# Optimization experiments

Hardware: AMD Instinct MI355X
Metric: run time of the kernel (lower is better)

The kernel has to match this reference:

```python
import jax, jax.numpy as jnp
import numpy as np

ALPHA = 0.2        # LeakyReLU negative slope
NEG_INF = -9e15    # mask value used by the torch module


def setup_inputs() -> dict:
    key = jax.random.key(0)
    ks = jax.random.split(key, 7)
    B, T, N, Cin = 4, 12, 1024, 64
    Fout, Em = 64, 16
    x = jax.random.normal(ks[0], (B, T, N, Cin), dtype=jnp.float32)
    adj = jax.random.randint(ks[1], (N, N), 0, 2, dtype=jnp.int32)
    emb1 = jax.random.normal(ks[2], (N, Em), dtype=jnp.float32)
    emb2 = jax.random.normal(ks[3], (N, Em), dtype=jnp.float32)
    W = jax.random.normal(ks[4], (Cin, Fout), dtype=jnp.float32) * (1.0 / np.sqrt(Cin))
    a = jax.random.normal(ks[5], (2 * Fout, 1), dtype=jnp.float32) * 0.1
    a2 = jax.random.normal(ks[6], (2 * Em, 1), dtype=jnp.float32) * 0.1
    return {"x": x, "adj": adj, "emb1": emb1, "emb2": emb2, "W": W, "a": a, "a2": a2}


def reference(x, adj, emb1, emb2, W, a, a2):
    B, T, N, Cin = x.shape
    Fout = W.shape[1]
    Em = emb1.shape[1]
    # Linear projection, fold batch*time: Wh [BT, N, Fout]
    Wh = jnp.einsum('btnc,cf->btnf', x, W).reshape(B * T, N, Fout)
    # Additive attention scores from node features
    s1 = Wh @ a[:Fout, 0]          # [BT, N]
    s2 = Wh @ a[Fout:, 0]          # [BT, N]
    e1 = s1[:, :, None] + s2[:, None, :]   # [BT, N, N]
    # Additive scores from static embeddings (shared across batch*time)
    f1 = emb1 @ a2[:Em, 0]         # [N]
    f2 = emb2 @ a2[Em:, 0]         # [N]
    e2 = f1[:, None] + f2[None, :]          # [N, N]
    e = jax.nn.leaky_relu(e1 + e2[None, :, :], negative_slope=ALPHA)
    # Adjacency mask + row softmax (dropout is inference no-op)
    att = jnp.where(adj[None, :, :] > 0, e, jnp.float32(NEG_INF))
    att = jax.nn.softmax(att, axis=-1)
    h_prime = att @ Wh                       # [BT, N, Fout]
    return jax.nn.elu(h_prime.reshape(B, T, N, Fout))
```

## Files before the change

### kernel.cpp

```cpp
#include <hip/hip_runtime.h>
#include <hip/hip_bf16.h>
#include <math.h>

#define BT 48
#define N 1024
#define F 64
#define CIN 64
#define EM 16
#define LRELU_A 0.2f
#define L2E 1.4426950408889634f

typedef short bf16x8 __attribute__((ext_vector_type(8)));
typedef float f32x4  __attribute__((ext_vector_type(4)));
typedef unsigned int u32x4 __attribute__((ext_vector_type(4)));

__device__ __forceinline__ unsigned short f2bf(float f) {
    unsigned int u = __float_as_uint(f);
    return (unsigned short)((u + 0x7FFFu + ((u >> 16) & 1u)) >> 16);
}

__global__ __launch_bounds__(256) void k_proj_misc(
    const float* __restrict__ x, const float* __restrict__ W,
    const float* __restrict__ a,
    const int* __restrict__ adj,
    const float* __restrict__ emb1, const float* __restrict__ emb2,
    const float* __restrict__ a2,
    unsigned short* __restrict__ WhSw,
    float* __restrict__ s1, float* __restrict__ s2,
    unsigned int* __restrict__ adjBits,
    float* __restrict__ f1, float* __restrict__ f2)
{
    const int tid = threadIdx.x;
    const int b   = blockIdx.x;

    __shared__ __align__(16) float sx[64 * 64];
    __shared__ __align__(16) float sWT[64 * 68];
    __shared__ __align__(16) unsigned short sT[64 * 80];

    const int bt  = b >> 4;
    const int n0  = (b & 15) * 64;
    const size_t grow = (size_t)bt * N + n0;

    {
        const float4* xv = (const float4*)(x + grow * CIN);
        float4* sxv = (float4*)sx;
        for (int i = tid; i < 64 * CIN / 4; i += 256) sxv[i] = xv[i];
        for (int i = tid; i < CIN * F; i += 256)
            sWT[(i & 63) * 68 + (i >> 6)] = W[i];
    }
    __syncthreads();

    const int f = tid & 63;
    const int w = tid >> 6;
    const float a1 = a[f], a2c = a[F + f];

    float acc[16];
#pragma unroll
    for (int t = 0; t < 16; ++t) acc[t] = 0.f;

    for (int cb = 0; cb < CIN; cb += 4) {
        const float4 wv = *(const float4*)&sWT[f * 68 + cb];
#pragma unroll
        for (int t = 0; t < 16; ++t) {
            const float4 xv = *(const float4*)&sx[(w * 16 + t) * 64 + cb];
            acc[t] = fmaf(xv.x, wv.x, acc[t]);
            acc[t] = fmaf(xv.y, wv.y, acc[t]);
            acc[t] = fmaf(xv.z, wv.z, acc[t]);
            acc[t] = fmaf(xv.w, wv.w, acc[t]);
        }
    }

#pragma unroll
    for (int t = 0; t < 16; ++t) {
        float v1 = acc[t] * a1;
        float v2 = acc[t] * a2c;
#pragma unroll
        for (int off = 32; off >= 1; off >>= 1) {
            v1 += __shfl_xor(v1, off, 64);
            v2 += __shfl_xor(v2, off, 64);
        }
        if (f == 0) {
            s1[grow + w * 16 + t] = v1;
            s2[grow + w * 16 + t] = v2;
        }
        sT[f * 80 + w * 16 + t] = f2bf(acc[t]);
    }
    __syncthreads();

    {
        const int ff = tid >> 2, qq = tid & 3;
        const int slot = (qq + ff) & 3;
        const int nb0 = (b & 15) * 2;
#pragma unroll
        for (int nbL = 0; nbL < 2; ++nbL) {
            const size_t dst = ((size_t)(bt * 32 + nb0 + nbL) * 64 + ff) * 32 + slot * 8;
            *(uint4*)&WhSw[dst] = *(const uint4*)&sT[ff * 80 + nbL * 32 + qq * 8];
        }
    }

    if (b < 128) {
        const int idx = b * 256 + tid;
        const int r = idx >> 5, w32 = idx & 31;
        const int* p = adj + (size_t)r * N + w32 * 32;
        unsigned int m = 0;
#pragma unroll
        for (int j = 0; j < 32; ++j) m |= (p[j] > 0 ? 1u : 0u) << j;
        adjBits[idx] = m;
    } else if (b < 132) {
        const int n = (b - 128) * 256 + tid;
        float v1 = 0.f, v2 = 0.f;
#pragma unroll
        for (int k = 0; k < EM; ++k) {
            v1 = fmaf(emb1[n * EM + k], a2[k], v1);
            v2 = fmaf(emb2[n * EM + k], a2[EM + k], v2);
        }
        f1[n] = v1; f2[n] = v2;
    }
}


#define PAIR(x1e, x1o, x2e, x2o, bit, dest) do {                           \
    float p0_ = fmaxf((x1e) * E1, (x2e) * E2);                             \
    float p1_ = fmaxf((x1o) * E1, (x2o) * E2);                             \
    p0_ = ((mb_ >> (bit)) & 1u) ? p0_ : 0.f;                               \
    p1_ = ((mb_ >> ((bit) + 1)) & 1u) ? p1_ : 0.f;                         \
    lsum += p0_ + p1_;                                                     \
    unsigned int pk_;                                                      \
    asm("v_cvt_pk_bf16_f32 %0, %1, %2" : "=v"(pk_) : "v"(p0_), "v"(p1_)); \
    dest = pk_;                                                            \
} while (0)

#define MAKE_ONE(ch, ks, Avar, abword) do {                                \
    const int jb_ = (ch) * 128 + (ks) * 32 + q * 8;                        \
    const float4 x1a_ = *(const float4*)&sX1[jb_];                         \
    const float4 x1b_ = *(const float4*)&sX1[jb_ + 4];                     \
    const float4 x2a_ = *(const float4*)&sX2[jb_];                         \
    const float4 x2b_ = *(const float4*)&sX2[jb_ + 4];                     \
    const unsigned int mb_ = ((abword) >> (q * 8)) & 0xFFu;                \
    unsigned int u0_, u1_, u2_, u3_;                                       \
    PAIR(x1a_.x, x1a_.y, x2a_.x, x2a_.y, 0, u0_);                          \
    PAIR(x1a_.z, x1a_.w, x2a_.z, x2a_.w, 2, u1_);                          \
    PAIR(x1b_.x, x1b_.y, x2b_.x, x2b_.y, 4, u2_);                          \
    PAIR(x1b_.z, x1b_.w, x2b_.z, x2b_.w, 6, u3_);                          \
    u32x4 av_; av_.x = u0_; av_.y = u1_; av_.z = u2_; av_.w = u3_;         \
    Avar = __builtin_bit_cast(bf16x8, av_);                                \
} while (0)

#define MAKE_AFR(ch, abv, A0, A1, A2, A3) do {                             \
    MAKE_ONE(ch, 0, A0, abv.x);                                            \
    MAKE_ONE(ch, 1, A1, abv.y);                                            \
    MAKE_ONE(ch, 2, A2, abv.z);                                            \
    MAKE_ONE(ch, 3, A3, abv.w);                                            \
} while (0)

#define LB(v, ch, ks, ct)                                                  \
    v = *(const bf16x8*)(gBc + (size_t)(ch) * 16384 + (ks) * 4096 +        \
        ((ct) * 16 + m15) * 64 + slotoff)

#define LOAD8(B0, B1, B2, B3, B4, B5, B6, B7, ch, ct0, ct1) do {           \
    LB(B0, ch, 0, ct0); LB(B1, ch, 1, ct0);                                \
    LB(B2, ch, 2, ct0); LB(B3, ch, 3, ct0);                                \
    LB(B4, ch, 0, ct1); LB(B5, ch, 1, ct1);                                \
    LB(B6, ch, 2, ct1); LB(B7, ch, 3, ct1);                                \
} while (0)

#define MFMA8(B0, B1, B2, B3, B4, B5, B6, B7, c0, c1) do {                 \
    acc##c0 = __builtin_amdgcn_mfma_f32_16x16x32_bf16(fA0, B0, acc##c0, 0, 0, 0); \
    acc##c0 = __builtin_amdgcn_mfma_f32_16x16x32_bf16(fA1, B1, acc##c0, 0, 0, 0); \
    acc##c0 = __builtin_amdgcn_mfma_f32_16x16x32_bf16(fA2, B2, acc##c0, 0, 0, 0); \
    acc##c0 = __builtin_amdgcn_mfma_f32_16x16x32_bf16(fA3, B3, acc##c0, 0, 0, 0); \
    acc##c1 = __builtin_amdgcn_mfma_f32_16x16x32_bf16(fA0, B4, acc##c1, 0, 0, 0); \
    acc##c1 = __builtin_amdgcn_mfma_f32_16x16x32_bf16(fA1, B5, acc##c1, 0, 0, 0); \
    acc##c1 = __builtin_amdgcn_mfma_f32_16x16x32_bf16(fA2, B6, acc##c1, 0, 0, 0); \
    acc##c1 = __builtin_amdgcn_mfma_f32_16x16x32_bf16(fA3, B7, acc##c1, 0, 0, 0); \
} while (0)

#define CHUNK_MID(ch) do {                                                 \
    LOAD8(Q0, Q1, Q2, Q3, Q4, Q5, Q6, Q7, ch, 2, 3);                       \
    const uint4 abv_ = abRow4[ch];                                         \
    MAKE_AFR(ch, abv_, fA0, fA1, fA2, fA3);                                \
    MFMA8(P0, P1, P2, P3, P4, P5, P6, P7, 0, 1);                           \
    LOAD8(P0, P1, P2, P3, P4, P5, P6, P7, (ch) + 1, 0, 1);                 \
    MFMA8(Q0, Q1, Q2, Q3, Q4, Q5, Q6, Q7, 2, 3);                           \
} while (0)

#define CHUNK_LAST(ch) do {                                                \
    LOAD8(Q0, Q1, Q2, Q3, Q4, Q5, Q6, Q7, ch, 2, 3);                       \
    const uint4 abv_ = abRow4[ch];                                         \
    MAKE_AFR(ch, abv_, fA0, fA1, fA2, fA3);                                \
    MFMA8(P0, P1, P2, P3, P4, P5, P6, P7, 0, 1);                           \
    MFMA8(Q0, Q1, Q2, Q3, Q4, Q5, Q6, Q7, 2, 3);                           \
} while (0)

#define EPI(ct, accv) do {                                                 \
    float h0_ = accv.x * rinv0, h1_ = accv.y * rinv1,                      \
          h2_ = accv.z * rinv2, h3_ = accv.w * rinv3;                      \
    h0_ = (h0_ > 0.f) ? h0_ : (__expf(h0_) - 1.f);                         \
    h1_ = (h1_ > 0.f) ? h1_ : (__expf(h1_) - 1.f);                         \
    h2_ = (h2_ > 0.f) ? h2_ : (__expf(h2_) - 1.f);                         \
    h3_ = (h3_ > 0.f) ? h3_ : (__expf(h3_) - 1.f);                         \
    float* op_ = out + (size_t)(bt * N + i0 + w * 16 + q * 4) * F          \
                 + (ct) * 16 + m15;                                        \
    op_[0 * F] = h0_; op_[1 * F] = h1_; op_[2 * F] = h2_; op_[3 * F] = h3_;\
} while (0)

__global__ __launch_bounds__(256, 3) void k_attn(
    const unsigned int* __restrict__ adjBits,
    const unsigned short* __restrict__ WhSw,
    const float* __restrict__ s1, const float* __restrict__ s2,
    const float* __restrict__ f1v, const float* __restrict__ f2v,
    float* __restrict__ out)
{
    __shared__ __align__(16) float sX1[N];
    __shared__ __align__(16) float sX2[N];
    __shared__ float sWmax[4];

    const int tid  = threadIdx.x;
    const int xcd = blockIdx.x & 7;
    const int idx = blockIdx.x >> 3;
    const int bt  = xcd * 6 + (idx >> 4);
    const int i0  = (idx & 15) * 64;
    const int lane = tid & 63;
    const int w    = tid >> 6;
    const int q    = lane >> 4;
    const int m15  = lane & 15;

    const int growq = i0 + w * 16 + m15;
    const uint4* abRow4 = (const uint4*)(adjBits + (size_t)growq * 32);
    const float rraw = s1[bt * N + growq] + f1v[growq];

    float cmax = -1e30f;
    for (int j = tid; j < N; j += 256) {
        const float c = (s2[bt * N + j] + f2v[j]) * L2E;
        sX1[j] = exp2f(c);
        sX2[j] = exp2f(LRELU_A * c);
        cmax = fmaxf(cmax, c);
    }
#pragma unroll
    for (int off = 32; off >= 1; off >>= 1) cmax = fmaxf(cmax, __shfl_xor(cmax, off, 64));
    if (lane == 0) sWmax[w] = cmax;
    __syncthreads();
    const float mx = fmaxf(fmaxf(sWmax[0], sWmax[1]), fmaxf(sWmax[2], sWmax[3]));

    const float r    = rraw * L2E;
    const float smx  = r + mx;
    const float mhat = fmaxf(smx, LRELU_A * smx);
    const float E1 = exp2f(r - mhat);
    const float E2 = exp2f(LRELU_A * r - mhat);
    float lsum = 0.f;

    const char* gBc = (const char*)(WhSw + (size_t)bt * 65536);
    const int slotoff = ((q + m15) & 3) * 16;

    f32x4 acc0 = 0.f, acc1 = 0.f, acc2 = 0.f, acc3 = 0.f;
    bf16x8 fA0, fA1, fA2, fA3;
    bf16x8 P0, P1, P2, P3, P4, P5, P6, P7;
    bf16x8 Q0, Q1, Q2, Q3, Q4, Q5, Q6, Q7;

    LOAD8(P0, P1, P2, P3, P4, P5, P6, P7, 0, 0, 1);

    CHUNK_MID(0); CHUNK_MID(1); CHUNK_MID(2); CHUNK_MID(3);
    CHUNK_MID(4); CHUNK_MID(5); CHUNK_MID(6); CHUNK_LAST(7);

    lsum += __shfl_xor(lsum, 16, 64);
    lsum += __shfl_xor(lsum, 32, 64);

    const float rinv0 = 1.f / __shfl(lsum, q * 4 + 0, 64);
    const float rinv1 = 1.f / __shfl(lsum, q * 4 + 1, 64);
    const float rinv2 = 1.f / __shfl(lsum, q * 4 + 2, 64);
    const float rinv3 = 1.f / __shfl(lsum, q * 4 + 3, 64);

    EPI(0, acc0); EPI(1, acc1); EPI(2, acc2); EPI(3, acc3);
}

extern "C" void kernel_launch(void* const* d_in, const int* in_sizes, int n_in,
                              void* d_out, int out_size, void* d_ws, size_t ws_size,
                              hipStream_t stream)
{
    const float* x    = (const float*)d_in[0];
    const int*   adj  = (const int*)  d_in[1];
    const float* emb1 = (const float*)d_in[2];
    const float* emb2 = (const float*)d_in[3];
    const float* W    = (const float*)d_in[4];
    const float* a    = (const float*)d_in[5];
    const float* a2   = (const float*)d_in[6];
    float* out = (float*)d_out;

    unsigned short* WhSw = (unsigned short*)d_ws;
    float* s1 = (float*)(WhSw + (size_t)BT * 65536);
    float* s2 = s1 + BT * N;
    float* f1 = s2 + BT * N;
    float* f2 = f1 + N;
    unsigned int* adjBits = (unsigned int*)(f2 + N);

    hipLaunchKernelGGL(k_proj_misc, dim3(768), dim3(256), 0, stream,
                       x, W, a, adj, emb1, emb2, a2, WhSw, s1, s2, adjBits, f1, f2);
    hipLaunchKernelGGL(k_attn, dim3(BT * 16), dim3(256), 0, stream,
                       adjBits, WhSw, s1, s2, f1, f2, out);
}
```

Measured before the change: 116.5 us.

## Register-tile projection GEMM with packed FP32 FMA and pack attention multiplies

The projection kernel now uses a 4x4 register tile per thread over a transposed, XOR-swizzled x tile in shared memory. It accumulates with v_pk_fma_f32, which cuts LDS traffic and the 64-lane shuffle reductions (now 16-lane) per output. The attention kernel's probability construction replaces scalar multiplies with v_pk_mul_f32 pairs. The cost is inline asm constraints and more scattered shared-memory stores into sT, which may bank-conflict.

```diff
diff --git a/kernel.cpp b/kernel.cpp
--- a/kernel.cpp
+++ b/kernel.cpp
@@ -12,12 +12,17 @@
 
 typedef short bf16x8 __attribute__((ext_vector_type(8)));
 typedef float f32x4  __attribute__((ext_vector_type(4)));
+typedef float f32x2  __attribute__((ext_vector_type(2)));
+typedef float f32x4e __attribute__((ext_vector_type(4)));
 typedef unsigned int u32x4 __attribute__((ext_vector_type(4)));
 
 __device__ __forceinline__ unsigned short f2bf(float f) {
     unsigned int u = __float_as_uint(f);
     return (unsigned short)((u + 0x7FFFu + ((u >> 16) & 1u)) >> 16);
 }
+
+#define PKFMA(acc, xp, wp) \
+    asm("v_pk_fma_f32 %0, %1, %2, %0" : "+v"(acc) : "v"(xp), "v"(wp))
 
 __global__ __launch_bounds__(256) void k_proj_misc(
     const float* __restrict__ x, const float* __restrict__ W,
@@ -33,8 +38,8 @@
     const int tid = threadIdx.x;
     const int b   = blockIdx.x;
 
-    __shared__ __align__(16) float sx[64 * 64];
-    __shared__ __align__(16) float sWT[64 * 68];
+    __shared__ __align__(16) float sxT[64 * 72];
+    __shared__ __align__(16) float sW[64 * 68];
     __shared__ __align__(16) unsigned short sT[64 * 80];
 
     const int bt  = b >> 4;
@@ -43,48 +48,79 @@
 
     {
         const float4* xv = (const float4*)(x + grow * CIN);
-        float4* sxv = (float4*)sx;
-        for (int i = tid; i < 64 * CIN / 4; i += 256) sxv[i] = xv[i];
-        for (int i = tid; i < CIN * F; i += 256)
-            sWT[(i & 63) * 68 + (i >> 6)] = W[i];
+        for (int i = tid; i < 1024; i += 256) {
+            const float4 v = xv[i];
+            const int row = i >> 4, c4 = (i & 15) * 4;
+            sxT[(c4 + 0) * 72 + (row ^ (((c4 + 0) & 15) << 2))] = v.x;
+            sxT[(c4 + 1) * 72 + (row ^ (((c4 + 1) & 15) << 2))] = v.y;
+            sxT[(c4 + 2) * 72 + (row ^ (((c4 + 2) & 15) << 2))] = v.z;
+            sxT[(c4 + 3) * 72 + (row ^ (((c4 + 3) & 15) << 2))] = v.w;
+        }
+        const float4* wv = (const float4*)W;
+        for (int i = tid; i < 1024; i += 256) {
+            const int k = i >> 4, c4 = (i & 15) * 4;
+            *(float4*)&sW[k * 68 + c4] = wv[i];
+        }
     }
     __syncthreads();
 
-    const int f = tid & 63;
-    const int w = tid >> 6;
-    const float a1 = a[f], a2c = a[F + f];
-
-    float acc[16];
-#pragma unroll
-    for (int t = 0; t < 16; ++t) acc[t] = 0.f;
-
-    for (int cb = 0; cb < CIN; cb += 4) {
-        const float4 wv = *(const float4*)&sWT[f * 68 + cb];
-#pragma unroll
-        for (int t = 0; t < 16; ++t) {
-            const float4 xv = *(const float4*)&sx[(w * 16 + t) * 64 + cb];
-            acc[t] = fmaf(xv.x, wv.x, acc[t]);
-            acc[t] = fmaf(xv.y, wv.y, acc[t]);
-            acc[t] = fmaf(xv.z, wv.z, acc[t]);
-            acc[t] = fmaf(xv.w, wv.w, acc[t]);
-        }
-    }
-
-#pragma unroll
-    for (int t = 0; t < 16; ++t) {
-        float v1 = acc[t] * a1;
-        float v2 = acc[t] * a2c;
-#pragma unroll
-        for (int off = 32; off >= 1; off >>= 1) {
-            v1 += __shfl_xor(v1, off, 64);
-            v2 += __shfl_xor(v2, off, 64);
-        }
-        if (f == 0) {
-            s1[grow + w * 16 + t] = v1;
-            s2[grow + w * 16 + t] = v2;
-        }
-        sT[f * 80 + w * 16 + t] = f2bf(acc[t]);
-    }
+    const int rg = tid >> 4, cg = tid & 15;
+    const int r0 = rg * 4, c0 = cg * 4;
+
+    f32x2 a00 = 0.f, a01 = 0.f, a10 = 0.f, a11 = 0.f;
+    f32x2 a20 = 0.f, a21 = 0.f, a30 = 0.f, a31 = 0.f;
+
+#pragma unroll
+    for (int k = 0; k < CIN; ++k) {
+        const float4 xr  = *(const float4*)&sxT[k * 72 + (r0 ^ ((k & 15) << 2))];
+        const float4 wv4 = *(const float4*)&sW[k * 68 + c0];
+        f32x2 w01; w01.x = wv4.x; w01.y = wv4.y;
+        f32x2 w23; w23.x = wv4.z; w23.y = wv4.w;
+        f32x2 xb;
+        xb.x = xr.x; xb.y = xr.x;
+        PKFMA(a00, xb, w01); PKFMA(a01, xb, w23);
+        xb.x = xr.y; xb.y = xr.y;
+        PKFMA(a10, xb, w01); PKFMA(a11, xb, w23);
+        xb.x = xr.z; xb.y = xr.z;
+        PKFMA(a20, xb, w01); PKFMA(a21, xb, w23);
+        xb.x = xr.w; xb.y = xr.w;
+        PKFMA(a30, xb, w01); PKFMA(a31, xb, w23);
+    }
+
+    {
+        const float4 aw1 = *(const float4*)&a[c0];
+        const float4 aw2 = *(const float4*)&a[F + c0];
+        float v1r0 = a00.x*aw1.x + a00.y*aw1.y + a01.x*aw1.z + a01.y*aw1.w;
+        float v1r1 = a10.x*aw1.x + a10.y*aw1.y + a11.x*aw1.z + a11.y*aw1.w;
+        float v1r2 = a20.x*aw1.x + a20.y*aw1.y + a21.x*aw1.z + a21.y*aw1.w;
+        float v1r3 = a30.x*aw1.x + a30.y*aw1.y + a31.x*aw1.z + a31.y*aw1.w;
+        float v2r0 = a00.x*aw2.x + a00.y*aw2.y + a01.x*aw2.z + a01.y*aw2.w;
+        float v2r1 = a10.x*aw2.x + a10.y*aw2.y + a11.x*aw2.z + a11.y*aw2.w;
+        float v2r2 = a20.x*aw2.x + a20.y*aw2.y + a21.x*aw2.z + a21.y*aw2.w;
+        float v2r3 = a30.x*aw2.x + a30.y*aw2.y + a31.x*aw2.z + a31.y*aw2.w;
+#pragma unroll
+        for (int off = 1; off <= 8; off <<= 1) {
+            v1r0 += __shfl_xor(v1r0, off, 64); v2r0 += __shfl_xor(v2r0, off, 64);
+            v1r1 += __shfl_xor(v1r1, off, 64); v2r1 += __shfl_xor(v2r1, off, 64);
+            v1r2 += __shfl_xor(v1r2, off, 64); v2r2 += __shfl_xor(v2r2, off, 64);
+            v1r3 += __shfl_xor(v1r3, off, 64); v2r3 += __shfl_xor(v2r3, off, 64);
+        }
+        if (cg == 0) {
+            s1[grow + r0 + 0] = v1r0; s2[grow + r0 + 0] = v2r0;
+            s1[grow + r0 + 1] = v1r1; s2[grow + r0 + 1] = v2r1;
+            s1[grow + r0 + 2] = v1r2; s2[grow + r0 + 2] = v2r2;
+            s1[grow + r0 + 3] = v1r3; s2[grow + r0 + 3] = v2r3;
+        }
+    }
+
+    sT[(c0+0)*80 + r0+0] = f2bf(a00.x); sT[(c0+1)*80 + r0+0] = f2bf(a00.y);
+    sT[(c0+2)*80 + r0+0] = f2bf(a01.x); sT[(c0+3)*80 + r0+0] = f2bf(a01.y);
+    sT[(c0+0)*80 + r0+1] = f2bf(a10.x); sT[(c0+1)*80 + r0+1] = f2bf(a10.y);
+    sT[(c0+2)*80 + r0+1] = f2bf(a11.x); sT[(c0+3)*80 + r0+1] = f2bf(a11.y);
+    sT[(c0+0)*80 + r0+2] = f2bf(a20.x); sT[(c0+1)*80 + r0+2] = f2bf(a20.y);
+    sT[(c0+2)*80 + r0+2] = f2bf(a21.x); sT[(c0+3)*80 + r0+2] = f2bf(a21.y);
+    sT[(c0+0)*80 + r0+3] = f2bf(a30.x); sT[(c0+1)*80 + r0+3] = f2bf(a30.y);
+    sT[(c0+2)*80 + r0+3] = f2bf(a31.x); sT[(c0+3)*80 + r0+3] = f2bf(a31.y);
     __syncthreads();
 
     {
@@ -119,9 +155,12 @@
 }
 
 
-#define PAIR(x1e, x1o, x2e, x2o, bit, dest) do {                           \
-    float p0_ = fmaxf((x1e) * E1, (x2e) * E2);                             \
-    float p1_ = fmaxf((x1o) * E1, (x2o) * E2);                             \
+#define PAIRPK(x1p, x2p, bit, dest) do {                                   \
+    f32x2 m1_, m2_;                                                        \
+    asm("v_pk_mul_f32 %0, %1, %2" : "=v"(m1_) : "v"(x1p), "v"(E1p));       \
+    asm("v_pk_mul_f32 %0, %1, %2" : "=v"(m2_) : "v"(x2p), "v"(E2p));       \
+    float p0_ = fmaxf(m1_.x, m2_.x);                                       \
+    float p1_ = fmaxf(m1_.y, m2_.y);                                       \
     p0_ = ((mb_ >> (bit)) & 1u) ? p0_ : 0.f;                               \
     p1_ = ((mb_ >> ((bit) + 1)) & 1u) ? p1_ : 0.f;                         \
     lsum += p0_ + p1_;                                                     \
@@ -132,16 +171,20 @@
 
 #define MAKE_ONE(ch, ks, Avar, abword) do {                                \
     const int jb_ = (ch) * 128 + (ks) * 32 + q * 8;                        \
-    const float4 x1a_ = *(const float4*)&sX1[jb_];                         \
-    const float4 x1b_ = *(const float4*)&sX1[jb_ + 4];                     \
-    const float4 x2a_ = *(const float4*)&sX2[jb_];                         \
-    const float4 x2b_ = *(const float4*)&sX2[jb_ + 4];                     \
+    const f32x4e x1a_ = *(const f32x4e*)&sX1[jb_];                         \
+    const f32x4e x1b_ = *(const f32x4e*)&sX1[jb_ + 4];                     \
+    const f32x4e x2a_ = *(const f32x4e*)&sX2[jb_];                         \
+    const f32x4e x2b_ = *(const f32x4e*)&sX2[jb_ + 4];                     \
     const unsigned int mb_ = ((abword) >> (q * 8)) & 0xFFu;                \
     unsigned int u0_, u1_, u2_, u3_;                                       \
-    PAIR(x1a_.x, x1a_.y, x2a_.x, x2a_.y, 0, u0_);                          \
-    PAIR(x1a_.z, x1a_.w, x2a_.z, x2a_.w, 2, u1_);                          \
-    PAIR(x1b_.x, x1b_.y, x2b_.x, x2b_.y, 4, u2_);                          \
-    PAIR(x1b_.z, x1b_.w, x2b_.z, x2b_.w, 6, u3_);                          \
+    PAIRPK(__builtin_shufflevector(x1a_, x1a_, 0, 1),                      \
+           __builtin_shufflevector(x2a_, x2a_, 0, 1), 0, u0_);             \
+    PAIRPK(__builtin_shufflevector(x1a_, x1a_, 2, 3),                      \
+           __builtin_shufflevector(x2a_, x2a_, 2, 3), 2, u1_);             \
+    PAIRPK(__builtin_shufflevector(x1b_, x1b_, 0, 1),                      \
+           __builtin_shufflevector(x2b_, x2b_, 0, 1), 4, u2_);             \
+    PAIRPK(__builtin_shufflevector(x1b_, x1b_, 2, 3),                      \
+           __builtin_shufflevector(x2b_, x2b_, 2, 3), 6, u3_);             \
     u32x4 av_; av_.x = u0_; av_.y = u1_; av_.z = u2_; av_.w = u3_;         \
     Avar = __builtin_bit_cast(bf16x8, av_);                                \
 } while (0)
@@ -247,6 +290,8 @@
     const float mhat = fmaxf(smx, LRELU_A * smx);
     const float E1 = exp2f(r - mhat);
     const float E2 = exp2f(LRELU_A * r - mhat);
+    f32x2 E1p; E1p.x = E1; E1p.y = E1;
+    f32x2 E2p; E2p.x = E2; E2p.y = E2;
     float lsum = 0.f;
 
     const char* gBc = (const char*)(WhSw + (size_t)bt * 65536);
```

Result: faster. 110.7 us (-5.0%).
